# Optimization experiments

Measured on AMD Instinct MI355X. Metric: run time of the kernel, lower is better.

Reference implementation:

```python
import jax, jax.numpy as jnp
import numpy as np

B, CIN, REL, OUT, SH, H, W = 8, 256, 16, 64, 8, 56, 56
HW = H * W
K = 7          # window size
DIL = 2        # dilation
EPS = 1e-5


def conv1x1(x, w, b=None):
    # x: [B,C,h,w], w: [O,C]
    y = jnp.einsum('oc,bchw->bohw', w, x)
    if b is not None:
        y = y + b[None, :, None, None]
    return y


def bn_eval(x, g, b, m, v):
    scale = g / jnp.sqrt(v + EPS)
    return x * scale[None, :, None, None] + (b - m * scale)[None, :, None, None]


def unfold49(x, pad_reflect, pad_zero):
    # x: [B,C,H,W] -> [B,C,49,H,W]; 7x7 window, dilation 2, stride 1.
    if pad_reflect:
        x = jnp.pad(x, ((0, 0), (0, 0), (pad_reflect, pad_reflect), (pad_reflect, pad_reflect)), mode='reflect')
    if pad_zero:
        x = jnp.pad(x, ((0, 0), (0, 0), (pad_zero, pad_zero), (pad_zero, pad_zero)))
    patches = [x[:, :, DIL * i:DIL * i + H, DIL * j:DIL * j + W]
               for i in range(K) for j in range(K)]
    return jnp.stack(patches, axis=2)


def setup_inputs() -> dict:
    key = jax.random.key(0)
    ks = jax.random.split(key, 12)
    s_in = 1.0 / np.sqrt(CIN)
    inp = {
        'x': jax.random.normal(ks[0], (B, CIN, H, W), jnp.float32),
        'w1': jax.random.normal(ks[1], (REL, CIN), jnp.float32) * s_in,
        'b1': jax.random.normal(ks[2], (REL,), jnp.float32) * 0.01,
        'w2': jax.random.normal(ks[3], (REL, CIN), jnp.float32) * s_in,
        'b2': jax.random.normal(ks[4], (REL,), jnp.float32) * 0.01,
        'w3': jax.random.normal(ks[5], (OUT, CIN), jnp.float32) * s_in,
        'b3': jax.random.normal(ks[6], (OUT,), jnp.float32) * 0.01,
        'bn1_g': jax.random.uniform(ks[7], (REL * (K * K + 1),), jnp.float32, 0.5, 1.5),
        'bn1_b': jax.random.normal(ks[8], (REL * (K * K + 1),), jnp.float32) * 0.01,
        'bn1_m': jnp.zeros((REL * (K * K + 1),), jnp.float32),
        'bn1_v': jnp.ones((REL * (K * K + 1),), jnp.float32),
        'wcw1': jax.random.normal(ks[9], (OUT // SH, REL * (K * K + 1)), jnp.float32) * (1.0 / np.sqrt(REL * 50)),
        'bn2_g': jax.random.uniform(ks[10], (OUT // SH,), jnp.float32, 0.5, 1.5),
        'bn2_b': jnp.zeros((OUT // SH,), jnp.float32),
        'bn2_m': jnp.zeros((OUT // SH,), jnp.float32),
        'bn2_v': jnp.ones((OUT // SH,), jnp.float32),
        'wcw2': jax.random.normal(ks[11], (K * K * OUT // SH, OUT // SH), jnp.float32) * (1.0 / np.sqrt(OUT // SH)),
        'bcw2': jnp.zeros((K * K * OUT // SH,), jnp.float32),
    }
    return inp


def reference(x, w1, b1, w2, b2, w3, b3, bn1_g, bn1_b, bn1_m, bn1_v,
              wcw1, bn2_g, bn2_b, bn2_m, bn2_v, wcw2, bcw2):
    x1 = conv1x1(x, w1, b1)                      # [B,REL,H,W]
    x2 = conv1x1(x, w2, b2)                      # [B,REL,H,W]
    x3 = conv1x1(x, w3, b3)                      # [B,OUT,H,W]

    # x1 -> [B,REL,1,HW]
    x1f = x1.reshape(B, REL, 1, HW)
    # x2: ReflectionPad2d(2) then Unfold(7, dilation=2, padding=4) -> [B,REL*49,1,HW]
    x2u = unfold49(x2, pad_reflect=2, pad_zero=4).reshape(B, REL * K * K, 1, HW)

    cat = jnp.concatenate([x1f, x2u], axis=1)    # [B, REL*50, 1, HW]
    t = jax.nn.relu(bn_eval(cat, bn1_g, bn1_b, bn1_m, bn1_v))
    t = conv1x1(t, wcw1)                         # [B, OUT/SH, 1, HW], no bias
    t = jax.nn.relu(bn_eval(t, bn2_g, bn2_b, bn2_m, bn2_v))
    wmap = conv1x1(t, wcw2, bcw2)                # [B, 49*OUT/SH, 1, HW]
    wmap = wmap.reshape(B, OUT // SH, K * K, HW)  # channel layout wc*49+k

    # Aggregation(7, 1, 6, 2, pad_mode=1): reflect-pad 6, 7x7 dilated unfold,
    # out[b,c,n] = sum_k unf[b,c,k,n] * w[b, c//SH, k, n]
    x3u = unfold49(x3, pad_reflect=6, pad_zero=0).reshape(B, OUT // SH, SH, K * K, HW)
    out = jnp.einsum('bgskn,bgkn->bgsn', x3u, wmap).reshape(B, OUT, H, W)
    return out
```

## Files before the change

### kernel.cpp

```cpp
#include <hip/hip_runtime.h>
#include <hip/hip_bf16.h>

#define HW    3136
#define HH    56
#define NCIN  256
#define MOUT  96
#define NREL  16
#define NOUT  64
#define NG    8
#define KK    49

#define OFF_WCAT  0
#define OFF_BCAT  24576
#define OFF_S1    24672
#define OFF_SH1   25472
#define OFF_WC1T  26272
#define OFF_B2F   32672
#define OFF_XCAT  32768
#define OFF_TBUF  2441216

__global__ __launch_bounds__(256) void kprep(
    const float* __restrict__ w1, const float* __restrict__ b1,
    const float* __restrict__ w2, const float* __restrict__ b2,
    const float* __restrict__ w3, const float* __restrict__ b3,
    const float* __restrict__ bn1g, const float* __restrict__ bn1b,
    const float* __restrict__ bn1m, const float* __restrict__ bn1v,
    const float* __restrict__ wcw1,
    const float* __restrict__ bn2g, const float* __restrict__ bn2b,
    const float* __restrict__ bn2m, const float* __restrict__ bn2v,
    float* __restrict__ ws)
{
    int idx = blockIdx.x * 256 + threadIdx.x;
    if (idx < 24576) {
        int o = idx >> 8, c = idx & 255;
        float v = (o < 16) ? w1[o * 256 + c]
                : (o < 32) ? w2[(o - 16) * 256 + c]
                           : w3[(o - 32) * 256 + c];
        ws[OFF_WCAT + idx] = v;
    }
    int i2 = idx - 24576;
    if (i2 >= 0 && i2 < 96) {
        float v = (i2 < 16) ? b1[i2] : (i2 < 32) ? b2[i2 - 16] : b3[i2 - 32];
        ws[OFF_BCAT + i2] = v;
    }
    int i3 = idx - 24672;
    if (i3 >= 0 && i3 < 800) {
        float s = bn1g[i3] / sqrtf(bn1v[i3] + 1e-5f);
        ws[OFF_S1 + i3]  = s;
        ws[OFF_SH1 + i3] = bn1b[i3] - bn1m[i3] * s;
    }
    int i4 = idx - 25472;
    if (i4 >= 0 && i4 < 6400) {
        int j = i4 >> 3, g = i4 & 7;
        float s2 = bn2g[g] / sqrtf(bn2v[g] + 1e-5f);
        ws[OFF_WC1T + i4] = wcw1[g * 800 + j] * s2;
    }
    int i5 = idx - 31872;
    if (i5 >= 0 && i5 < 8) {
        float s2 = bn2g[i5] / sqrtf(bn2v[i5] + 1e-5f);
        ws[OFF_B2F + i5] = bn2b[i5] - bn2m[i5] * s2;
    }
}

__global__ __launch_bounds__(256) void kconvA(
    const float* __restrict__ x, const float* __restrict__ wcat,
    const float* __restrict__ bcat, float* __restrict__ xcat)
{
    __shared__ float wl[64][100];
    __shared__ float xl[64][64];
    const int tid = threadIdx.x;
    const int bi  = blockIdx.x;
    const int b   = bi / 49;
    const int hw0 = (bi % 49) * 64;
    const int pxp = tid & 31;
    const int og  = tid >> 5;
    const int obase = og * 12;

    float acc0[12], acc1[12];
#pragma unroll
    for (int o = 0; o < 12; ++o) {
        float bv = bcat[obase + o];
        acc0[o] = bv; acc1[o] = bv;
    }

    const float* xb = x + (size_t)b * NCIN * HW + hw0;

    for (int cc = 0; cc < 4; ++cc) {
        __syncthreads();
#pragma unroll
        for (int t = 0; t < 24; ++t) {
            int idx = t * 256 + tid;
            int o = idx >> 6;
            int c = idx & 63;
            wl[c][o] = wcat[o * NCIN + cc * 64 + c];
        }
#pragma unroll
        for (int i = 0; i < 16; ++i) {
            int c = i * 4 + (tid >> 6);
            xl[c][tid & 63] = xb[(size_t)(cc * 64 + c) * HW + (tid & 63)];
        }
        __syncthreads();
#pragma unroll 4
        for (int c = 0; c < 64; ++c) {
            float xv0 = xl[c][pxp];
            float xv1 = xl[c][pxp + 32];
            float wv[12];
            *(float4*)&wv[0] = *(const float4*)&wl[c][obase];
            *(float4*)&wv[4] = *(const float4*)&wl[c][obase + 4];
            *(float4*)&wv[8] = *(const float4*)&wl[c][obase + 8];
#pragma unroll
            for (int o = 0; o < 12; ++o) {
                acc0[o] = fmaf(xv0, wv[o], acc0[o]);
                acc1[o] = fmaf(xv1, wv[o], acc1[o]);
            }
        }
    }

    float* outp = xcat + (size_t)b * MOUT * HW + hw0;
#pragma unroll
    for (int o = 0; o < 12; ++o) {
        outp[(size_t)(obase + o) * HW + pxp]      = acc0[o];
        outp[(size_t)(obase + o) * HW + pxp + 32] = acc1[o];
    }
}

__device__ __forceinline__ int refl(int p) {
    return p < 0 ? -p : (p > 55 ? 110 - p : p);
}

__global__ __launch_bounds__(512) void kwmap_t(
    const float* __restrict__ xcat, const float* __restrict__ s1,
    const float* __restrict__ sh1, const float* __restrict__ wc1t,
    const float* __restrict__ b2f, float* __restrict__ tbuf)
{
    __shared__ float red[8][8][64];
    const int tid = threadIdx.x;
    const int w   = tid >> 6;
    const int l   = tid & 63;
    const int pxg = blockIdx.x * 64;
    const int b   = pxg / HW;
    const int nb  = pxg - b * HW;
    const int n   = nb + l;
    const int y   = n / HH;
    const int xx  = n - y * HH;

    const float* x1 = xcat + (size_t)b * MOUT * HW;
    const float* x2 = x1 + 16 * HW;

    float acc[8];
#pragma unroll
    for (int g = 0; g < 8; ++g) acc[g] = 0.f;

    const int u0 = (50 * w) >> 3;
    const int u1 = (50 * (w + 1)) >> 3;

#pragma unroll 1
    for (int u = u0; u < u1; ++u) {
        if (u == 0) {
#pragma unroll
            for (int r = 0; r < 16; ++r) {
                float v = x1[r * HW + n];
                v = fmaxf(fmaf(v, s1[r], sh1[r]), 0.f);
                const float* wr = wc1t + r * 8;
#pragma unroll
                for (int g = 0; g < 8; ++g) acc[g] = fmaf(v, wr[g], acc[g]);
            }
        } else {
            const int kk = __builtin_amdgcn_readfirstlane(u - 1);
            const int i  = kk / 7;
            const int jj = kk - i * 7;
            int p = y + 2 * i - 6;
            int q = xx + 2 * jj - 6;
            bool z = (p < -2) | (p > 57) | (q < -2) | (q > 57);
            int off = refl(p) * HH + refl(q);
            const float* x2o = x2 + off;
#pragma unroll
            for (int r = 0; r < 16; ++r) {
                const int j = 16 + r * KK + kk;
                float v = z ? 0.f : x2o[(size_t)r * HW];
                v = fmaxf(fmaf(v, s1[j], sh1[j]), 0.f);
                const float* wr = wc1t + j * 8;
#pragma unroll
                for (int g = 0; g < 8; ++g) acc[g] = fmaf(v, wr[g], acc[g]);
            }
        }
    }

#pragma unroll
    for (int g = 0; g < 8; ++g) red[w][g][l] = acc[g];
    __syncthreads();

    {
        const int g  = tid >> 6;
        const int px = tid & 63;
        float s = b2f[g];
#pragma unroll
        for (int ww = 0; ww < 8; ++ww) s += red[ww][g][px];
        s = fmaxf(s, 0.f);
        tbuf[((size_t)b * 8 + g) * HW + nb + px] = s;
    }
}

__global__ __launch_bounds__(256) void kaggr(
    const float* __restrict__ xcat, const float* __restrict__ tbuf,
    const float* __restrict__ wcw2, const float* __restrict__ bcw2,
    float* __restrict__ out)
{
    const int n = blockIdx.x * 256 + threadIdx.x;
    if (n >= HW) return;
    const int g = blockIdx.y;
    const int b = blockIdx.z;
    const int y  = n / HH;
    const int xx = n - y * HH;

    const float* x3 = xcat + ((size_t)b * MOUT + 32 + g * 8) * HW;

    float t[8];
#pragma unroll
    for (int e = 0; e < 8; ++e) t[e] = tbuf[((size_t)b * 8 + e) * HW + n];

    float acc[8];
#pragma unroll
    for (int s = 0; s < 8; ++s) acc[s] = 0.f;

    const float* wrow = wcw2 + (size_t)g * KK * 8;
    const float* brow = bcw2 + g * KK;

#pragma unroll 1
    for (int i = 0; i < 7; ++i) {
        int p  = y + 2 * i - 6;
        int py = refl(p);
#pragma unroll
        for (int jj = 0; jj < 7; ++jj) {
            int q  = xx + 2 * jj - 6;
            int px = refl(q);
            int off = py * HH + px;
            int k   = i * 7 + jj;
            float wv = brow[k];
#pragma unroll
            for (int e = 0; e < 8; ++e) wv = fmaf(t[e], wrow[k * 8 + e], wv);
#pragma unroll
            for (int s = 0; s < 8; ++s)
                acc[s] = fmaf(x3[s * HW + off], wv, acc[s]);
        }
    }

    float* op = out + ((size_t)b * NOUT + g * 8) * HW + n;
#pragma unroll
    for (int s = 0; s < 8; ++s) op[s * HW] = acc[s];
}

extern "C" void kernel_launch(void* const* d_in, const int* in_sizes, int n_in,
                              void* d_out, int out_size, void* d_ws, size_t ws_size,
                              hipStream_t stream) {
    const float* x    = (const float*)d_in[0];
    const float* w1   = (const float*)d_in[1];
    const float* b1   = (const float*)d_in[2];
    const float* w2   = (const float*)d_in[3];
    const float* b2   = (const float*)d_in[4];
    const float* w3   = (const float*)d_in[5];
    const float* b3   = (const float*)d_in[6];
    const float* bn1g = (const float*)d_in[7];
    const float* bn1b = (const float*)d_in[8];
    const float* bn1m = (const float*)d_in[9];
    const float* bn1v = (const float*)d_in[10];
    const float* wcw1 = (const float*)d_in[11];
    const float* bn2g = (const float*)d_in[12];
    const float* bn2b = (const float*)d_in[13];
    const float* bn2m = (const float*)d_in[14];
    const float* bn2v = (const float*)d_in[15];
    const float* wcw2 = (const float*)d_in[16];
    const float* bcw2 = (const float*)d_in[17];

    float* ws = (float*)d_ws;
    float* wcat = ws + OFF_WCAT;
    float* bcat = ws + OFF_BCAT;
    float* s1   = ws + OFF_S1;
    float* sh1  = ws + OFF_SH1;
    float* wc1t = ws + OFF_WC1T;
    float* b2f  = ws + OFF_B2F;
    float* xcat = ws + OFF_XCAT;
    float* tbuf = ws + OFF_TBUF;

    kprep<<<125, 256, 0, stream>>>(w1, b1, w2, b2, w3, b3,
                                   bn1g, bn1b, bn1m, bn1v, wcw1,
                                   bn2g, bn2b, bn2m, bn2v, ws);
    kconvA<<<392, 256, 0, stream>>>(x, wcat, bcat, xcat);
    kwmap_t<<<392, 512, 0, stream>>>(xcat, s1, sh1, wc1t, b2f, tbuf);
    dim3 gC(13, 8, 8);
    kaggr<<<gC, 256, 0, stream>>>(xcat, tbuf, wcw2, bcw2, (float*)d_out);
}
```

Before: 86.62 us.

## Fuse prep, weight-map and aggregation kernels; fold parameter prep into consumers

Drops the separate prep kernel: the conv kernel reads w1/w2/w3 and biases directly, and the fused kernel computes the BN scales and folded wcw1 into shared memory per block. The weight-map reduction and the aggregation run in one kernel, so the intermediate t buffer stays in LDS instead of making a global round trip, and two launches go away. The conv kernel is also retiled to one pixel by 24 outputs per thread. The trade-off is that every block recomputes the ~30KB of BN/weight folding, larger LDS use may limit occupancy, and aggregation now runs on only 392 blocks of 512 threads.

```diff
diff --git a/kernel.cpp b/kernel.cpp
--- a/kernel.cpp
+++ b/kernel.cpp
@@ -5,135 +5,91 @@
 #define HH    56
 #define NCIN  256
 #define MOUT  96
-#define NREL  16
-#define NOUT  64
-#define NG    8
 #define KK    49
 
-#define OFF_WCAT  0
-#define OFF_BCAT  24576
-#define OFF_S1    24672
-#define OFF_SH1   25472
-#define OFF_WC1T  26272
-#define OFF_B2F   32672
-#define OFF_XCAT  32768
-#define OFF_TBUF  2441216
-
-__global__ __launch_bounds__(256) void kprep(
+#define OFF_XCAT  0
+
+__device__ __forceinline__ int refl(int p) {
+    return p < 0 ? -p : (p > 55 ? 110 - p : p);
+}
+
+__global__ __launch_bounds__(256) void kconv(
+    const float* __restrict__ x,
     const float* __restrict__ w1, const float* __restrict__ b1,
     const float* __restrict__ w2, const float* __restrict__ b2,
     const float* __restrict__ w3, const float* __restrict__ b3,
+    float* __restrict__ xcat)
+{
+    __shared__ float wl[64][100];
+    __shared__ float xl[64][64];
+    const int tid = threadIdx.x;
+    const int b   = blockIdx.x / 49;
+    const int hw0 = (blockIdx.x % 49) * 64;
+    const int l   = tid & 63;
+    const int og  = tid >> 6;
+    const int ob  = og * 24;
+
+    float acc[24];
+#pragma unroll
+    for (int oo = 0; oo < 24; ++oo) {
+        int o = ob + oo;
+        acc[oo] = (o < 16) ? b1[o] : (o < 32) ? b2[o - 16] : b3[o - 32];
+    }
+
+    const float* xb = x + (size_t)b * NCIN * HW + hw0;
+
+    for (int cc = 0; cc < 4; ++cc) {
+        __syncthreads();
+#pragma unroll
+        for (int t = 0; t < 24; ++t) {
+            int idx = t * 256 + tid;
+            int o = idx >> 6, c = idx & 63;
+            const float* src = (o < 16) ? w1 + o * 256
+                             : (o < 32) ? w2 + (o - 16) * 256
+                                        : w3 + (o - 32) * 256;
+            wl[c][o] = src[cc * 64 + c];
+        }
+#pragma unroll
+        for (int i = 0; i < 16; ++i) {
+            int c = i * 4 + og;
+            xl[c][l] = xb[(size_t)(cc * 64 + c) * HW + l];
+        }
+        __syncthreads();
+#pragma unroll 2
+        for (int c = 0; c < 64; ++c) {
+            float xv = xl[c][l];
+            float wv[24];
+#pragma unroll
+            for (int q = 0; q < 6; ++q)
+                *(float4*)&wv[q * 4] = *(const float4*)&wl[c][ob + q * 4];
+#pragma unroll
+            for (int oo = 0; oo < 24; ++oo)
+                acc[oo] = fmaf(xv, wv[oo], acc[oo]);
+        }
+    }
+
+    float* outp = xcat + (size_t)b * MOUT * HW + hw0;
+#pragma unroll
+    for (int oo = 0; oo < 24; ++oo)
+        outp[(size_t)(ob + oo) * HW + l] = acc[oo];
+}
+
+__global__ __launch_bounds__(512) void kfused(
+    const float* __restrict__ xcat,
     const float* __restrict__ bn1g, const float* __restrict__ bn1b,
     const float* __restrict__ bn1m, const float* __restrict__ bn1v,
     const float* __restrict__ wcw1,
     const float* __restrict__ bn2g, const float* __restrict__ bn2b,
     const float* __restrict__ bn2m, const float* __restrict__ bn2v,
-    float* __restrict__ ws)
+    const float* __restrict__ wcw2, const float* __restrict__ bcw2,
+    float* __restrict__ out)
 {
-    int idx = blockIdx.x * 256 + threadIdx.x;
-    if (idx < 24576) {
-        int o = idx >> 8, c = idx & 255;
-        float v = (o < 16) ? w1[o * 256 + c]
-                : (o < 32) ? w2[(o - 16) * 256 + c]
-                           : w3[(o - 32) * 256 + c];
-        ws[OFF_WCAT + idx] = v;
-    }
-    int i2 = idx - 24576;
-    if (i2 >= 0 && i2 < 96) {
-        float v = (i2 < 16) ? b1[i2] : (i2 < 32) ? b2[i2 - 16] : b3[i2 - 32];
-        ws[OFF_BCAT + i2] = v;
-    }
-    int i3 = idx - 24672;
-    if (i3 >= 0 && i3 < 800) {
-        float s = bn1g[i3] / sqrtf(bn1v[i3] + 1e-5f);
-        ws[OFF_S1 + i3]  = s;
-        ws[OFF_SH1 + i3] = bn1b[i3] - bn1m[i3] * s;
-    }
-    int i4 = idx - 25472;
-    if (i4 >= 0 && i4 < 6400) {
-        int j = i4 >> 3, g = i4 & 7;
-        float s2 = bn2g[g] / sqrtf(bn2v[g] + 1e-5f);
-        ws[OFF_WC1T + i4] = wcw1[g * 800 + j] * s2;
-    }
-    int i5 = idx - 31872;
-    if (i5 >= 0 && i5 < 8) {
-        float s2 = bn2g[i5] / sqrtf(bn2v[i5] + 1e-5f);
-        ws[OFF_B2F + i5] = bn2b[i5] - bn2m[i5] * s2;
-    }
-}
-
-__global__ __launch_bounds__(256) void kconvA(
-    const float* __restrict__ x, const float* __restrict__ wcat,
-    const float* __restrict__ bcat, float* __restrict__ xcat)
-{
-    __shared__ float wl[64][100];
-    __shared__ float xl[64][64];
-    const int tid = threadIdx.x;
-    const int bi  = blockIdx.x;
-    const int b   = bi / 49;
-    const int hw0 = (bi % 49) * 64;
-    const int pxp = tid & 31;
-    const int og  = tid >> 5;
-    const int obase = og * 12;
-
-    float acc0[12], acc1[12];
-#pragma unroll
-    for (int o = 0; o < 12; ++o) {
-        float bv = bcat[obase + o];
-        acc0[o] = bv; acc1[o] = bv;
-    }
-
-    const float* xb = x + (size_t)b * NCIN * HW + hw0;
-
-    for (int cc = 0; cc < 4; ++cc) {
-        __syncthreads();
-#pragma unroll
-        for (int t = 0; t < 24; ++t) {
-            int idx = t * 256 + tid;
-            int o = idx >> 6;
-            int c = idx & 63;
-            wl[c][o] = wcat[o * NCIN + cc * 64 + c];
-        }
-#pragma unroll
-        for (int i = 0; i < 16; ++i) {
-            int c = i * 4 + (tid >> 6);
-            xl[c][tid & 63] = xb[(size_t)(cc * 64 + c) * HW + (tid & 63)];
-        }
-        __syncthreads();
-#pragma unroll 4
-        for (int c = 0; c < 64; ++c) {
-            float xv0 = xl[c][pxp];
-            float xv1 = xl[c][pxp + 32];
-            float wv[12];
-            *(float4*)&wv[0] = *(const float4*)&wl[c][obase];
-            *(float4*)&wv[4] = *(const float4*)&wl[c][obase + 4];
-            *(float4*)&wv[8] = *(const float4*)&wl[c][obase + 8];
-#pragma unroll
-            for (int o = 0; o < 12; ++o) {
-                acc0[o] = fmaf(xv0, wv[o], acc0[o]);
-                acc1[o] = fmaf(xv1, wv[o], acc1[o]);
-            }
-        }
-    }
-
-    float* outp = xcat + (size_t)b * MOUT * HW + hw0;
-#pragma unroll
-    for (int o = 0; o < 12; ++o) {
-        outp[(size_t)(obase + o) * HW + pxp]      = acc0[o];
-        outp[(size_t)(obase + o) * HW + pxp + 32] = acc1[o];
-    }
-}
-
-__device__ __forceinline__ int refl(int p) {
-    return p < 0 ? -p : (p > 55 ? 110 - p : p);
-}
-
-__global__ __launch_bounds__(512) void kwmap_t(
-    const float* __restrict__ xcat, const float* __restrict__ s1,
-    const float* __restrict__ sh1, const float* __restrict__ wc1t,
-    const float* __restrict__ b2f, float* __restrict__ tbuf)
-{
+    __shared__ float s1l[800], sh1l[800];
+    __shared__ float wc1tl[800][8];
     __shared__ float red[8][8][64];
+    __shared__ float tl[8][64];
+    __shared__ float b2fl[8];
+
     const int tid = threadIdx.x;
     const int w   = tid >> 6;
     const int l   = tid & 63;
@@ -144,6 +100,22 @@
     const int y   = n / HH;
     const int xx  = n - y * HH;
 
+    for (int i = tid; i < 800; i += 512) {
+        float s = bn1g[i] / sqrtf(bn1v[i] + 1e-5f);
+        s1l[i]  = s;
+        sh1l[i] = bn1b[i] - bn1m[i] * s;
+    }
+    for (int i = tid; i < 6400; i += 512) {
+        int j = i >> 3, g = i & 7;
+        float s2 = bn2g[g] / sqrtf(bn2v[g] + 1e-5f);
+        wc1tl[j][g] = wcw1[g * 800 + j] * s2;
+    }
+    if (tid < 8) {
+        float s2 = bn2g[tid] / sqrtf(bn2v[tid] + 1e-5f);
+        b2fl[tid] = bn2b[tid] - bn2m[tid] * s2;
+    }
+    __syncthreads();
+
     const float* x1 = xcat + (size_t)b * MOUT * HW;
     const float* x2 = x1 + 16 * HW;
 
@@ -160,10 +132,13 @@
 #pragma unroll
             for (int r = 0; r < 16; ++r) {
                 float v = x1[r * HW + n];
-                v = fmaxf(fmaf(v, s1[r], sh1[r]), 0.f);
-                const float* wr = wc1t + r * 8;
-#pragma unroll
-                for (int g = 0; g < 8; ++g) acc[g] = fmaf(v, wr[g], acc[g]);
+                v = fmaxf(fmaf(v, s1l[r], sh1l[r]), 0.f);
+                float4 wa = *(const float4*)&wc1tl[r][0];
+                float4 wb = *(const float4*)&wc1tl[r][4];
+                acc[0] = fmaf(v, wa.x, acc[0]); acc[1] = fmaf(v, wa.y, acc[1]);
+                acc[2] = fmaf(v, wa.z, acc[2]); acc[3] = fmaf(v, wa.w, acc[3]);
+                acc[4] = fmaf(v, wb.x, acc[4]); acc[5] = fmaf(v, wb.y, acc[5]);
+                acc[6] = fmaf(v, wb.z, acc[6]); acc[7] = fmaf(v, wb.w, acc[7]);
             }
         } else {
             const int kk = __builtin_amdgcn_readfirstlane(u - 1);
@@ -178,10 +153,13 @@
             for (int r = 0; r < 16; ++r) {
                 const int j = 16 + r * KK + kk;
                 float v = z ? 0.f : x2o[(size_t)r * HW];
-                v = fmaxf(fmaf(v, s1[j], sh1[j]), 0.f);
-                const float* wr = wc1t + j * 8;
-#pragma unroll
-                for (int g = 0; g < 8; ++g) acc[g] = fmaf(v, wr[g], acc[g]);
+                v = fmaxf(fmaf(v, s1l[j], sh1l[j]), 0.f);
+                float4 wa = *(const float4*)&wc1tl[j][0];
+                float4 wb = *(const float4*)&wc1tl[j][4];
+                acc[0] = fmaf(v, wa.x, acc[0]); acc[1] = fmaf(v, wa.y, acc[1]);
+                acc[2] = fmaf(v, wa.z, acc[2]); acc[3] = fmaf(v, wa.w, acc[3]);
+                acc[4] = fmaf(v, wb.x, acc[4]); acc[5] = fmaf(v, wb.y, acc[5]);
+                acc[6] = fmaf(v, wb.z, acc[6]); acc[7] = fmaf(v, wb.w, acc[7]);
             }
         }
     }
@@ -189,42 +167,28 @@
 #pragma unroll
     for (int g = 0; g < 8; ++g) red[w][g][l] = acc[g];
     __syncthreads();
-
     {
         const int g  = tid >> 6;
         const int px = tid & 63;
-        float s = b2f[g];
+        float s = b2fl[g];
 #pragma unroll
         for (int ww = 0; ww < 8; ++ww) s += red[ww][g][px];
-        s = fmaxf(s, 0.f);
-        tbuf[((size_t)b * 8 + g) * HW + nb + px] = s;
-    }
-}
-
-__global__ __launch_bounds__(256) void kaggr(
-    const float* __restrict__ xcat, const float* __restrict__ tbuf,
-    const float* __restrict__ wcw2, const float* __restrict__ bcw2,
-    float* __restrict__ out)
-{
-    const int n = blockIdx.x * 256 + threadIdx.x;
-    if (n >= HW) return;
-    const int g = blockIdx.y;
-    const int b = blockIdx.z;
-    const int y  = n / HH;
-    const int xx = n - y * HH;
-
-    const float* x3 = xcat + ((size_t)b * MOUT + 32 + g * 8) * HW;
-
+        tl[g][px] = fmaxf(s, 0.f);
+    }
+    __syncthreads();
+
+    const int g = __builtin_amdgcn_readfirstlane(tid >> 6);
     float t[8];
 #pragma unroll
-    for (int e = 0; e < 8; ++e) t[e] = tbuf[((size_t)b * 8 + e) * HW + n];
-
-    float acc[8];
-#pragma unroll
-    for (int s = 0; s < 8; ++s) acc[s] = 0.f;
-
+    for (int e = 0; e < 8; ++e) t[e] = tl[e][l];
+
+    const float* x3   = xcat + ((size_t)b * MOUT + 32 + g * 8) * HW;
     const float* wrow = wcw2 + (size_t)g * KK * 8;
-    const float* brow = bcw2 + g * KK;
+    const float* brow = bcw2 + (size_t)g * KK;
+
+    float acc2[8];
+#pragma unroll
+    for (int s = 0; s < 8; ++s) acc2[s] = 0.f;
 
 #pragma unroll 1
     for (int i = 0; i < 7; ++i) {
@@ -241,13 +205,13 @@
             for (int e = 0; e < 8; ++e) wv = fmaf(t[e], wrow[k * 8 + e], wv);
 #pragma unroll
             for (int s = 0; s < 8; ++s)
-                acc[s] = fmaf(x3[s * HW + off], wv, acc[s]);
-        }
-    }
-
-    float* op = out + ((size_t)b * NOUT + g * 8) * HW + n;
-#pragma unroll
-    for (int s = 0; s < 8; ++s) op[s * HW] = acc[s];
+                acc2[s] = fmaf(x3[(size_t)s * HW + off], wv, acc2[s]);
+        }
+    }
+
+    float* op = out + ((size_t)b * 64 + g * 8) * HW + n;
+#pragma unroll
+    for (int s = 0; s < 8; ++s) op[(size_t)s * HW] = acc2[s];
 }
 
 extern "C" void kernel_launch(void* const* d_in, const int* in_sizes, int n_in,
@@ -272,21 +236,10 @@
     const float* wcw2 = (const float*)d_in[16];
     const float* bcw2 = (const float*)d_in[17];
 
-    float* ws = (float*)d_ws;
-    float* wcat = ws + OFF_WCAT;
-    float* bcat = ws + OFF_BCAT;
-    float* s1   = ws + OFF_S1;
-    float* sh1  = ws + OFF_SH1;
-    float* wc1t = ws + OFF_WC1T;
-    float* b2f  = ws + OFF_B2F;
-    float* xcat = ws + OFF_XCAT;
-    float* tbuf = ws + OFF_TBUF;
-
-    kprep<<<125, 256, 0, stream>>>(w1, b1, w2, b2, w3, b3,
-                                   bn1g, bn1b, bn1m, bn1v, wcw1,
-                                   bn2g, bn2b, bn2m, bn2v, ws);
-    kconvA<<<392, 256, 0, stream>>>(x, wcat, bcat, xcat);
-    kwmap_t<<<392, 512, 0, stream>>>(xcat, s1, sh1, wc1t, b2f, tbuf);
-    dim3 gC(13, 8, 8);
-    kaggr<<<gC, 256, 0, stream>>>(xcat, tbuf, wcw2, bcw2, (float*)d_out);
-}
+    float* xcat = (float*)d_ws + OFF_XCAT;
+
+    kconv<<<392, 256, 0, stream>>>(x, w1, b1, w2, b2, w3, b3, xcat);
+    kfused<<<392, 512, 0, stream>>>(xcat, bn1g, bn1b, bn1m, bn1v, wcw1,
+                                    bn2g, bn2b, bn2m, bn2v, wcw2, bcw2,
+                                    (float*)d_out);
+}
```

After: 112.7 us. 1.3x slower.

## Fuse wmap reduction with aggregation and restructure 1x1 conv weight access

Applied to the files above, without the earlier changes.

Merges the kernel that computes the bottleneck feature t with the aggregation kernel, so t stays in shared memory instead of going through a global buffer and an extra launch. Each block now covers 32 pixels, with half-wavefronts splitting the reduction channels and the output sub-channels. The 1x1 conv kernel now reads pre-transposed weights straight from global memory (wave-uniform, cached) instead of staging them in LDS, and uses 512 threads with one pixel per thread. The cost is more blocks, each redoing work on fewer pixels, and lower ILP per thread in the conv.

```diff
diff --git a/kernel.cpp b/kernel.cpp
--- a/kernel.cpp
+++ b/kernel.cpp
@@ -5,19 +5,19 @@
 #define HH    56
 #define NCIN  256
 #define MOUT  96
-#define NREL  16
-#define NOUT  64
-#define NG    8
 #define KK    49
 
-#define OFF_WCAT  0
+#define OFF_WT    0
 #define OFF_BCAT  24576
 #define OFF_S1    24672
 #define OFF_SH1   25472
 #define OFF_WC1T  26272
 #define OFF_B2F   32672
 #define OFF_XCAT  32768
-#define OFF_TBUF  2441216
+
+__device__ __forceinline__ int refl(int p) {
+    return p < 0 ? -p : (p > 55 ? 110 - p : p);
+}
 
 __global__ __launch_bounds__(256) void kprep(
     const float* __restrict__ w1, const float* __restrict__ b1,
@@ -36,7 +36,7 @@
         float v = (o < 16) ? w1[o * 256 + c]
                 : (o < 32) ? w2[(o - 16) * 256 + c]
                            : w3[(o - 32) * 256 + c];
-        ws[OFF_WCAT + idx] = v;
+        ws[OFF_WT + c * 96 + o] = v;
     }
     int i2 = idx - 24576;
     if (i2 >= 0 && i2 < 96) {
@@ -62,90 +62,77 @@
     }
 }
 
-__global__ __launch_bounds__(256) void kconvA(
-    const float* __restrict__ x, const float* __restrict__ wcat,
+__global__ __launch_bounds__(512) void kconv(
+    const float* __restrict__ x, const float* __restrict__ wT,
     const float* __restrict__ bcat, float* __restrict__ xcat)
 {
-    __shared__ float wl[64][100];
     __shared__ float xl[64][64];
     const int tid = threadIdx.x;
-    const int bi  = blockIdx.x;
-    const int b   = bi / 49;
-    const int hw0 = (bi % 49) * 64;
-    const int pxp = tid & 31;
-    const int og  = tid >> 5;
-    const int obase = og * 12;
-
-    float acc0[12], acc1[12];
-#pragma unroll
-    for (int o = 0; o < 12; ++o) {
-        float bv = bcat[obase + o];
-        acc0[o] = bv; acc1[o] = bv;
-    }
+    const int l   = tid & 63;
+    const int wv  = __builtin_amdgcn_readfirstlane(tid >> 6);
+    const int b   = blockIdx.x / 49;
+    const int hw0 = (blockIdx.x % 49) * 64;
+    const int ob  = wv * 12;
+
+    float acc[12];
+    const float* bc = bcat + ob;
+#pragma unroll
+    for (int i = 0; i < 12; ++i) acc[i] = bc[i];
 
     const float* xb = x + (size_t)b * NCIN * HW + hw0;
 
     for (int cc = 0; cc < 4; ++cc) {
         __syncthreads();
 #pragma unroll
-        for (int t = 0; t < 24; ++t) {
-            int idx = t * 256 + tid;
-            int o = idx >> 6;
-            int c = idx & 63;
-            wl[c][o] = wcat[o * NCIN + cc * 64 + c];
+        for (int i = 0; i < 8; ++i)
+            xl[i * 8 + wv][l] = xb[(size_t)(cc * 64 + i * 8 + wv) * HW + l];
+        __syncthreads();
+
+        const float* wp = wT + (cc * 64) * 96 + ob;
+#pragma unroll 4
+        for (int k = 0; k < 64; ++k) {
+            float xv = xl[k][l];
+            const float4* wq = (const float4*)(wp + k * 96);
+            float4 A = wq[0], B = wq[1], C = wq[2];
+            acc[0]  = fmaf(xv, A.x, acc[0]);  acc[1]  = fmaf(xv, A.y, acc[1]);
+            acc[2]  = fmaf(xv, A.z, acc[2]);  acc[3]  = fmaf(xv, A.w, acc[3]);
+            acc[4]  = fmaf(xv, B.x, acc[4]);  acc[5]  = fmaf(xv, B.y, acc[5]);
+            acc[6]  = fmaf(xv, B.z, acc[6]);  acc[7]  = fmaf(xv, B.w, acc[7]);
+            acc[8]  = fmaf(xv, C.x, acc[8]);  acc[9]  = fmaf(xv, C.y, acc[9]);
+            acc[10] = fmaf(xv, C.z, acc[10]); acc[11] = fmaf(xv, C.w, acc[11]);
         }
-#pragma unroll
-        for (int i = 0; i < 16; ++i) {
-            int c = i * 4 + (tid >> 6);
-            xl[c][tid & 63] = xb[(size_t)(cc * 64 + c) * HW + (tid & 63)];
-        }
-        __syncthreads();
-#pragma unroll 4
-        for (int c = 0; c < 64; ++c) {
-            float xv0 = xl[c][pxp];
-            float xv1 = xl[c][pxp + 32];
-            float wv[12];
-            *(float4*)&wv[0] = *(const float4*)&wl[c][obase];
-            *(float4*)&wv[4] = *(const float4*)&wl[c][obase + 4];
-            *(float4*)&wv[8] = *(const float4*)&wl[c][obase + 8];
-#pragma unroll
-            for (int o = 0; o < 12; ++o) {
-                acc0[o] = fmaf(xv0, wv[o], acc0[o]);
-                acc1[o] = fmaf(xv1, wv[o], acc1[o]);
-            }
-        }
     }
 
     float* outp = xcat + (size_t)b * MOUT * HW + hw0;
 #pragma unroll
-    for (int o = 0; o < 12; ++o) {
-        outp[(size_t)(obase + o) * HW + pxp]      = acc0[o];
-        outp[(size_t)(obase + o) * HW + pxp + 32] = acc1[o];
-    }
-}
-
-__device__ __forceinline__ int refl(int p) {
-    return p < 0 ? -p : (p > 55 ? 110 - p : p);
-}
-
-__global__ __launch_bounds__(512) void kwmap_t(
-    const float* __restrict__ xcat, const float* __restrict__ s1,
-    const float* __restrict__ sh1, const float* __restrict__ wc1t,
-    const float* __restrict__ b2f, float* __restrict__ tbuf)
+    for (int i = 0; i < 12; ++i)
+        outp[(size_t)(ob + i) * HW + l] = acc[i];
+}
+
+__global__ __launch_bounds__(512) void kmain(
+    const float* __restrict__ xcat,
+    const float* __restrict__ s1, const float* __restrict__ sh1,
+    const float* __restrict__ wc1t, const float* __restrict__ b2f,
+    const float* __restrict__ wcw2, const float* __restrict__ bcw2,
+    float* __restrict__ out)
 {
-    __shared__ float red[8][8][64];
+    __shared__ float red[16][8][32];
+    __shared__ float tl[8][32];
+
     const int tid = threadIdx.x;
     const int w   = tid >> 6;
     const int l   = tid & 63;
-    const int pxg = blockIdx.x * 64;
-    const int b   = pxg / HW;
-    const int nb  = pxg - b * HW;
-    const int n   = nb + l;
+    const int px  = l & 31;
+    const int rh  = l >> 5;
+    const int b   = blockIdx.x / 98;
+    const int nb  = (blockIdx.x % 98) * 32;
+    const int n   = nb + px;
     const int y   = n / HH;
     const int xx  = n - y * HH;
 
     const float* x1 = xcat + (size_t)b * MOUT * HW;
     const float* x2 = x1 + 16 * HW;
+    const int rb = rh * 8;
 
     float acc[8];
 #pragma unroll
@@ -158,12 +145,16 @@
     for (int u = u0; u < u1; ++u) {
         if (u == 0) {
 #pragma unroll
-            for (int r = 0; r < 16; ++r) {
+            for (int rr = 0; rr < 8; ++rr) {
+                int r = rb + rr;
                 float v = x1[r * HW + n];
                 v = fmaxf(fmaf(v, s1[r], sh1[r]), 0.f);
-                const float* wr = wc1t + r * 8;
-#pragma unroll
-                for (int g = 0; g < 8; ++g) acc[g] = fmaf(v, wr[g], acc[g]);
+                const float4* wq = (const float4*)(wc1t + r * 8);
+                float4 A = wq[0], Bv = wq[1];
+                acc[0] = fmaf(v, A.x, acc[0]);  acc[1] = fmaf(v, A.y, acc[1]);
+                acc[2] = fmaf(v, A.z, acc[2]);  acc[3] = fmaf(v, A.w, acc[3]);
+                acc[4] = fmaf(v, Bv.x, acc[4]); acc[5] = fmaf(v, Bv.y, acc[5]);
+                acc[6] = fmaf(v, Bv.z, acc[6]); acc[7] = fmaf(v, Bv.w, acc[7]);
             }
         } else {
             const int kk = __builtin_amdgcn_readfirstlane(u - 1);
@@ -173,58 +164,45 @@
             int q = xx + 2 * jj - 6;
             bool z = (p < -2) | (p > 57) | (q < -2) | (q > 57);
             int off = refl(p) * HH + refl(q);
-            const float* x2o = x2 + off;
-#pragma unroll
-            for (int r = 0; r < 16; ++r) {
-                const int j = 16 + r * KK + kk;
-                float v = z ? 0.f : x2o[(size_t)r * HW];
+#pragma unroll
+            for (int rr = 0; rr < 8; ++rr) {
+                int r = rb + rr;
+                int j = 16 + r * KK + kk;
+                float v = z ? 0.f : x2[(size_t)r * HW + off];
                 v = fmaxf(fmaf(v, s1[j], sh1[j]), 0.f);
-                const float* wr = wc1t + j * 8;
-#pragma unroll
-                for (int g = 0; g < 8; ++g) acc[g] = fmaf(v, wr[g], acc[g]);
+                const float4* wq = (const float4*)(wc1t + j * 8);
+                float4 A = wq[0], Bv = wq[1];
+                acc[0] = fmaf(v, A.x, acc[0]);  acc[1] = fmaf(v, A.y, acc[1]);
+                acc[2] = fmaf(v, A.z, acc[2]);  acc[3] = fmaf(v, A.w, acc[3]);
+                acc[4] = fmaf(v, Bv.x, acc[4]); acc[5] = fmaf(v, Bv.y, acc[5]);
+                acc[6] = fmaf(v, Bv.z, acc[6]); acc[7] = fmaf(v, Bv.w, acc[7]);
             }
         }
     }
 
 #pragma unroll
-    for (int g = 0; g < 8; ++g) red[w][g][l] = acc[g];
+    for (int g = 0; g < 8; ++g) red[w * 2 + rh][g][px] = acc[g];
     __syncthreads();
 
-    {
-        const int g  = tid >> 6;
-        const int px = tid & 63;
+    if (tid < 256) {
+        int g = tid >> 5, p2 = tid & 31;
         float s = b2f[g];
 #pragma unroll
-        for (int ww = 0; ww < 8; ++ww) s += red[ww][g][px];
-        s = fmaxf(s, 0.f);
-        tbuf[((size_t)b * 8 + g) * HW + nb + px] = s;
-    }
-}
-
-__global__ __launch_bounds__(256) void kaggr(
-    const float* __restrict__ xcat, const float* __restrict__ tbuf,
-    const float* __restrict__ wcw2, const float* __restrict__ bcw2,
-    float* __restrict__ out)
-{
-    const int n = blockIdx.x * 256 + threadIdx.x;
-    if (n >= HW) return;
-    const int g = blockIdx.y;
-    const int b = blockIdx.z;
-    const int y  = n / HH;
-    const int xx = n - y * HH;
-
-    const float* x3 = xcat + ((size_t)b * MOUT + 32 + g * 8) * HW;
-
+        for (int sl = 0; sl < 16; ++sl) s += red[sl][g][p2];
+        tl[g][p2] = fmaxf(s, 0.f);
+    }
+    __syncthreads();
+
+    const int g  = __builtin_amdgcn_readfirstlane(w);
     float t[8];
 #pragma unroll
-    for (int e = 0; e < 8; ++e) t[e] = tbuf[((size_t)b * 8 + e) * HW + n];
-
-    float acc[8];
-#pragma unroll
-    for (int s = 0; s < 8; ++s) acc[s] = 0.f;
-
+    for (int e = 0; e < 8; ++e) t[e] = tl[e][px];
+
+    const float* x3   = xcat + ((size_t)b * MOUT + 32 + g * 8 + rh * 4) * HW;
     const float* wrow = wcw2 + (size_t)g * KK * 8;
-    const float* brow = bcw2 + g * KK;
+    const float* brow = bcw2 + (size_t)g * KK;
+
+    float a2[4] = {0.f, 0.f, 0.f, 0.f};
 
 #pragma unroll 1
     for (int i = 0; i < 7; ++i) {
@@ -233,21 +211,22 @@
 #pragma unroll
         for (int jj = 0; jj < 7; ++jj) {
             int q  = xx + 2 * jj - 6;
-            int px = refl(q);
-            int off = py * HH + px;
+            int qx = refl(q);
+            int off = py * HH + qx;
             int k   = i * 7 + jj;
-            float wv = brow[k];
-#pragma unroll
-            for (int e = 0; e < 8; ++e) wv = fmaf(t[e], wrow[k * 8 + e], wv);
-#pragma unroll
-            for (int s = 0; s < 8; ++s)
-                acc[s] = fmaf(x3[s * HW + off], wv, acc[s]);
+            float wvv = brow[k];
+            const float* wr = wrow + k * 8;
+#pragma unroll
+            for (int e = 0; e < 8; ++e) wvv = fmaf(t[e], wr[e], wvv);
+#pragma unroll
+            for (int s = 0; s < 4; ++s)
+                a2[s] = fmaf(x3[(size_t)s * HW + off], wvv, a2[s]);
         }
     }
 
-    float* op = out + ((size_t)b * NOUT + g * 8) * HW + n;
-#pragma unroll
-    for (int s = 0; s < 8; ++s) op[s * HW] = acc[s];
+    float* op = out + ((size_t)b * 64 + g * 8 + rh * 4) * HW + n;
+#pragma unroll
+    for (int s = 0; s < 4; ++s) op[(size_t)s * HW] = a2[s];
 }
 
 extern "C" void kernel_launch(void* const* d_in, const int* in_sizes, int n_in,
@@ -273,20 +252,13 @@
     const float* bcw2 = (const float*)d_in[17];
 
     float* ws = (float*)d_ws;
-    float* wcat = ws + OFF_WCAT;
-    float* bcat = ws + OFF_BCAT;
-    float* s1   = ws + OFF_S1;
-    float* sh1  = ws + OFF_SH1;
-    float* wc1t = ws + OFF_WC1T;
-    float* b2f  = ws + OFF_B2F;
-    float* xcat = ws + OFF_XCAT;
-    float* tbuf = ws + OFF_TBUF;
 
     kprep<<<125, 256, 0, stream>>>(w1, b1, w2, b2, w3, b3,
                                    bn1g, bn1b, bn1m, bn1v, wcw1,
                                    bn2g, bn2b, bn2m, bn2v, ws);
-    kconvA<<<392, 256, 0, stream>>>(x, wcat, bcat, xcat);
-    kwmap_t<<<392, 512, 0, stream>>>(xcat, s1, sh1, wc1t, b2f, tbuf);
-    dim3 gC(13, 8, 8);
-    kaggr<<<gC, 256, 0, stream>>>(xcat, tbuf, wcw2, bcw2, (float*)d_out);
-}
+    kconv<<<392, 512, 0, stream>>>(x, ws + OFF_WT, ws + OFF_BCAT,
+                                   ws + OFF_XCAT);
+    kmain<<<784, 512, 0, stream>>>(ws + OFF_XCAT, ws + OFF_S1, ws + OFF_SH1,
+                                   ws + OFF_WC1T, ws + OFF_B2F, wcw2, bcw2,
+                                   (float*)d_out);
+}
```

Measured after the change: 95.97 us. +10.8%, slower.
